# Optimization experiments

Hardware: AMD Instinct MI355X
Metric: run time of the kernel (lower is better)

Reference implementation:

```python
import jax, jax.numpy as jnp
import numpy as np

B, N, D, FF, L = 32, 1000, 128, 512, 6
EPS = 1e-5  # InstanceNorm1d default eps


def _inorm(x, g, b):
    # InstanceNorm1d on [B, d, N] == normalize over sequence dim N per channel (biased var)
    m = jnp.mean(x, axis=1, keepdims=True)
    v = jnp.var(x, axis=1, keepdims=True)
    return (x - m) / jnp.sqrt(v + EPS) * g + b


def setup_inputs() -> dict:
    key = jax.random.key(0)
    ks = jax.random.split(key, 10)
    s = 0.05
    data = jax.random.normal(ks[0], (B, N, 2), dtype=jnp.float32)
    # negative pairwise distances (module calls it negative_dist)
    dist = -jax.random.uniform(ks[1], (B, N, N), dtype=jnp.float32)
    log_scale = jnp.ones((1,), dtype=jnp.float32)
    We = jax.random.normal(ks[2], (D, 2), dtype=jnp.float32) * s
    be = jnp.zeros((D,), dtype=jnp.float32)
    Wq = jax.random.normal(ks[3], (L, D, D), dtype=jnp.float32) * s
    Wk = jax.random.normal(ks[4], (L, D, D), dtype=jnp.float32) * s
    Wv = jax.random.normal(ks[5], (L, D, D), dtype=jnp.float32) * s
    g1 = jnp.ones((L, D), dtype=jnp.float32)
    b1 = jnp.zeros((L, D), dtype=jnp.float32)
    W1 = jax.random.normal(ks[6], (L, FF, D), dtype=jnp.float32) * s
    bw1 = jnp.zeros((L, FF), dtype=jnp.float32)
    W2 = jax.random.normal(ks[7], (L, D, FF), dtype=jnp.float32) * s
    bw2 = jnp.zeros((L, D), dtype=jnp.float32)
    g2 = jnp.ones((L, D), dtype=jnp.float32)
    b2 = jnp.zeros((L, D), dtype=jnp.float32)
    alpha = jnp.ones((L,), dtype=jnp.float32)  # AFT_dist_alpha per layer
    return dict(data=data, dist=dist, log_scale=log_scale, We=We, be=be,
                Wq=Wq, Wk=Wk, Wv=Wv, g1=g1, b1=b1, W1=W1, bw1=bw1,
                W2=W2, bw2=bw2, g2=g2, b2=b2, alpha=alpha)


def reference(data, dist, log_scale, We, be, Wq, Wk, Wv, g1, b1, W1, bw1, W2, bw2, g2, b2, alpha):
    x = data @ We.T + be  # [B,N,D]
    for i in range(L):
        q = x @ Wq[i].T
        k = x @ Wk[i].T
        v = x @ Wv[i].T
        A = jnp.exp(log_scale[0] * alpha[i] * dist)  # [B,N,N]
        ek = jnp.exp(k)
        bias = jnp.einsum('bnm,bmd->bnd', A, ek * v)
        denom = jnp.einsum('bnm,bmd->bnd', A, ek)
        out = jax.nn.sigmoid(q) * (bias / denom)
        x1 = _inorm(x + out, g1[i], b1[i])
        h = jax.nn.relu(x1 @ W1[i].T + bw1[i]) @ W2[i].T + bw2[i]
        x = _inorm(x1 + h, g2[i], b2[i])
    return x
```

## Files before the change

### kernel.cpp

```cpp
#include <hip/hip_runtime.h>
#include <hip/hip_bf16.h>

typedef __attribute__((ext_vector_type(4))) float f32x4;
typedef __attribute__((ext_vector_type(8))) short bf16x8;
typedef __attribute__((ext_vector_type(4))) short s16x4;

#define LCOUNT 6

static __device__ __forceinline__ unsigned short f2b(float f){
  __hip_bfloat16 h = __float2bfloat16(f);
  return __builtin_bit_cast(unsigned short, h);
}
static __device__ __forceinline__ float b2f(unsigned short u){
  unsigned int x = ((unsigned int)u) << 16;
  return __builtin_bit_cast(float, x);
}
static __device__ __forceinline__ void gl16(const void* g, void* l){
  __builtin_amdgcn_global_load_lds(
      (const __attribute__((address_space(1))) void*)g,
      (__attribute__((address_space(3))) void*)l, 16, 0, 0);
}
static __device__ __forceinline__ f32x4 mfma16(bf16x8 a, bf16x8 b, f32x4 c){
  return __builtin_amdgcn_mfma_f32_16x16x32_bf16(a, b, c, 0, 0, 0);
}

__global__ void k_cvt5(const float* __restrict__ Wq, const float* __restrict__ Wk,
                       const float* __restrict__ Wv, const float* __restrict__ W1,
                       const float* __restrict__ W2,
                       unsigned short* __restrict__ wqb, unsigned short* __restrict__ wkb,
                       unsigned short* __restrict__ wvb, unsigned short* __restrict__ w1b,
                       unsigned short* __restrict__ w2b){
  int i = blockIdx.x*256 + threadIdx.x;
  if (i < 98304) wqb[i] = f2b(Wq[i]);
  else if (i < 196608) wkb[i-98304] = f2b(Wk[i-98304]);
  else if (i < 294912) wvb[i-196608] = f2b(Wv[i-196608]);
  else if (i < 688128) w1b[i-294912] = f2b(W1[i-294912]);
  else w2b[i-688128] = f2b(W2[i-688128]);
}

__global__ void k_cvtdist(const float* __restrict__ dist, unsigned short* __restrict__ db){
  int t = blockIdx.x*256 + threadIdx.x;
  int row = t >> 7, ch = t & 127;
  bf16x8 w;
  if (ch >= 125){
#pragma unroll
    for (int e=0;e<8;e++) w[e] = 0;
  } else {
    const float* p = dist + (size_t)row*1000 + ch*8;
    f32x4 a = *(const f32x4*)p;
    f32x4 b = *(const f32x4*)(p + 4);
#pragma unroll
    for (int e=0;e<4;e++){ w[e] = (short)f2b(a[e]); w[4+e] = (short)f2b(b[e]); }
  }
  *(bf16x8*)&db[(size_t)row*1024 + ch*8] = w;
}

__global__ void k_embed(const float* __restrict__ data, const float* __restrict__ We,
                        const float* __restrict__ be, float* __restrict__ x,
                        unsigned short* __restrict__ xb){
  int idx = blockIdx.x*256 + threadIdx.x;
  int d = idx & 127, bn = idx >> 7;
  float v = data[bn*2]*We[d*2] + data[bn*2+1]*We[d*2+1] + be[d];
  x[idx] = v; xb[idx] = f2b(v);
}

__global__ __launch_bounds__(256) void k_napply(
  const float* __restrict__ src, const float* __restrict__ part, int cnt,
  const float* __restrict__ g, const float* __restrict__ beta,
  float* __restrict__ dstf, unsigned short* __restrict__ dstb,
  float* __restrict__ dout)
{
  __shared__ float sna[128], snc[128];
  int blk = blockIdx.x, tid = threadIdx.x;
  int b = blk / 125;
  if (tid < 128){
    float s1 = 0.f, s2 = 0.f;
    for (int c = 0; c < cnt; ++c){
      size_t pi = (((size_t)b*cnt + c)*128 + tid)*2;
      s1 += part[pi]; s2 += part[pi+1];
    }
    float mean = s1 * 1e-3f;
    float var  = s2 * 1e-3f - mean*mean;
    float a = g[tid] * rsqrtf(var + 1e-5f);
    sna[tid] = a; snc[tid] = beta[tid] - mean*a;
  }
  __syncthreads();
  size_t base = (size_t)blk*1024 + tid*4;
  f32x4 v = *(const f32x4*)&src[base];
  int d0 = (tid*4) & 127;
  f32x4 o; s16x4 ob;
#pragma unroll
  for (int e=0;e<4;e++){
    o[e] = v[e]*sna[d0+e] + snc[d0+e];
    ob[e] = (short)f2b(o[e]);
  }
  *(f32x4*)&dstf[base] = o;
  *(s16x4*)&dstb[base] = ob;
  if (dout) *(f32x4*)&dout[base] = o;
}

__global__ __launch_bounds__(256) void k_qkv(
  const unsigned short* __restrict__ xb,
  const unsigned short* __restrict__ Wqb, const unsigned short* __restrict__ Wkb,
  const unsigned short* __restrict__ Wvb,
  unsigned short* __restrict__ sigq, unsigned short* __restrict__ Zc)
{
  __shared__ unsigned short LA[2][4][64][8];
  __shared__ unsigned short LB[2][4][256][8];
  int tid = threadIdx.x, wid = tid>>6, lane = tid&63;
  int l15 = lane&15, lg = lane>>4;
  int wm = wid>>1, wn = wid&1;
  int bt = blockIdx.x, b = bt>>4, t = bt&15;
  int kv = blockIdx.y;
  int lrow = t*64 + lane; if (lrow > 999) lrow = 999;
  size_t arow = (size_t)(b*1000 + lrow);

  f32x4 zf = {0.f,0.f,0.f,0.f};
  f32x4 acc[2][4], acc2[2][4];
#pragma unroll
  for (int i=0;i<2;i++)
#pragma unroll
    for (int j=0;j<4;j++){ acc[i][j] = zf; acc2[i][j] = zf; }

  auto stage = [&](int kk, int buf){
    int k0 = kk*32;
    gl16(xb + arow*128 + k0 + wid*8, &LA[buf][wid][0][0]);
    if (kv == 0){
#pragma unroll
      for (int t2=0;t2<2;++t2){
        int e = wid + t2*4, g2 = e>>1, nb = e&1;
        gl16(Wqb + (size_t)(nb*64+lane)*128 + k0 + g2*8, &LB[buf][g2][nb*64][0]);
      }
    } else {
#pragma unroll
      for (int t2=0;t2<4;++t2){
        int e = wid + t2*4, g2 = e&3, nb = e>>2;
        const unsigned short* src = (nb < 2)
          ? Wkb + (size_t)(nb*64+lane)*128 + k0 + g2*8
          : Wvb + (size_t)((nb-2)*64+lane)*128 + k0 + g2*8;
        gl16(src, &LB[buf][g2][nb*64][0]);
      }
    }
  };
  auto compute = [&](int buf){
    bf16x8 af[2];
#pragma unroll
    for (int i=0;i<2;i++) af[i] = *(const bf16x8*)&LA[buf][lg][wm*32 + i*16 + l15][0];
#pragma unroll
    for (int j=0;j<4;j++){
      bf16x8 bq = *(const bf16x8*)&LB[buf][lg][wn*64 + j*16 + l15][0];
#pragma unroll
      for (int i=0;i<2;i++) acc[i][j] = mfma16(af[i], bq, acc[i][j]);
      if (kv){
        bf16x8 bv = *(const bf16x8*)&LB[buf][lg][128 + wn*64 + j*16 + l15][0];
#pragma unroll
        for (int i=0;i<2;i++) acc2[i][j] = mfma16(af[i], bv, acc2[i][j]);
      }
    }
  };

  stage(0, 0);
  __syncthreads();
  for (int kk = 0; kk < 4; ++kk){
    int buf = kk & 1;
    if (kk < 3) stage(kk+1, buf^1);
    compute(buf);
    __syncthreads();
  }

#pragma unroll
  for (int i=0;i<2;i++){
    int m4 = t*64 + wm*32 + i*16 + lg*4;
    if (m4 >= 1000) continue;
#pragma unroll
    for (int j=0;j<4;j++){
      int col = wn*64 + j*16 + l15;
      if (kv == 0){
#pragma unroll
        for (int r=0;r<4;r++)
          sigq[(size_t)(b*1000 + m4 + r)*128 + col] = f2b(1.f/(1.f + __expf(-acc[i][j][r])));
      } else {
        s16x4 pv, pk;
#pragma unroll
        for (int r=0;r<4;r++){
          float ek = __expf(acc[i][j][r]);
          pk[r] = (short)f2b(ek);
          pv[r] = (short)f2b(ek * acc2[i][j][r]);
        }
        size_t base = ((size_t)(b*128 + (m4>>3))*256 + col)*8 + ((m4>>2)&1)*4;
        *(s16x4*)&Zc[base] = pv;
        *(s16x4*)&Zc[base + 1024] = pk;
      }
    }
  }
}

template<int USE16>
__global__ __launch_bounds__(256) void k_attn(
  const float* __restrict__ dist, const unsigned short* __restrict__ db16,
  const unsigned short* __restrict__ Zc, const unsigned short* __restrict__ sigq,
  float* __restrict__ x, float* __restrict__ partA,
  const float* __restrict__ log_scale, const float* __restrict__ alpha, int layer)
{
  union SM {
    struct { unsigned short A[2][4][64][8]; unsigned short B[2][4][256][8]; } st;
    float den[64][128];
  };
  __shared__ SM sm;
  int tid = threadIdx.x, wid = tid>>6, lane = tid&63;
  int l15 = lane&15, lg = lane>>4;
  int bb = blockIdx.y, t = blockIdx.x, n0 = t*64;
  float sc = log_scale[0]*alpha[layer];
  const unsigned short* Zb = Zc + ((size_t)bb << 18);
  int arow = tid>>2, ag = tid&3;
  int an = n0 + arow; if (an > 999) an = 999;
  const size_t drow = (size_t)(bb*1000 + an);

  f32x4 zf = {0.f,0.f,0.f,0.f};
  f32x4 acc[4][4];
#pragma unroll
  for (int i=0;i<4;i++)
#pragma unroll
    for (int j=0;j<4;j++) acc[i][j] = zf;

  auto issueB = [&](int kk, int buf){
#pragma unroll
    for (int t2=0;t2<4;++t2){
      int e = wid + t2*4, g2 = e&3, cb = e>>2;
      gl16(Zb + ((size_t)((kk*4 + g2)*256 + cb*64 + lane))*8, &sm.st.B[buf][g2][cb*64][0]);
    }
  };
  auto loadA = [&](int kk, float* v){
    int k0 = kk*32 + ag*8;
    if (USE16){
      bf16x8 r = *(const bf16x8*)(db16 + drow*1024 + k0);
#pragma unroll
      for (int e=0;e<8;e++) v[e] = b2f((unsigned short)r[e]);
    } else {
      const float* dp = dist + (size_t)drow*1000;
      if (k0 + 8 <= 1000){
        f32x4 a0 = *(const f32x4*)(dp + k0);
        f32x4 a1 = *(const f32x4*)(dp + k0 + 4);
#pragma unroll
        for (int e=0;e<4;e++){ v[e] = a0[e]; v[4+e] = a1[e]; }
      } else {
#pragma unroll
        for (int e=0;e<8;e++){
          int m = k0 + e; if (m > 999) m = 999;
          v[e] = dp[m];
        }
      }
    }
  };
  auto expwrite = [&](const float* v, int buf){
    bf16x8 w;
#pragma unroll
    for (int e=0;e<8;e++) w[e] = (short)f2b(__expf(sc*v[e]));
    *(bf16x8*)&sm.st.A[buf][ag][arow][0] = w;
  };
  auto compute = [&](int buf){
    bf16x8 af[4], bq[4];
#pragma unroll
    for (int i=0;i<4;i++) af[i] = *(const bf16x8*)&sm.st.A[buf][lg][i*16 + l15][0];
#pragma unroll
    for (int j=0;j<4;j++) bq[j] = *(const bf16x8*)&sm.st.B[buf][lg][wid*64 + j*16 + l15][0];
#pragma unroll
    for (int i=0;i<4;i++)
#pragma unroll
      for (int j=0;j<4;j++)
        acc[i][j] = mfma16(af[i], bq[j], acc[i][j]);
  };

  float av[8];
  issueB(0, 0);
  loadA(0, av);
  expwrite(av, 0);
  __syncthreads();
  for (int kk = 0; kk < 32; ++kk){
    int buf = kk & 1;
    float nv[8];
    if (kk < 31){ issueB(kk+1, buf^1); loadA(kk+1, nv); }
    compute(buf);
    if (kk < 31) expwrite(nv, buf^1);
    __syncthreads();
  }

  if (wid >= 2){
#pragma unroll
    for (int i=0;i<4;i++)
#pragma unroll
      for (int j=0;j<4;j++){
        int dcol = (wid-2)*64 + j*16 + l15;
#pragma unroll
        for (int r=0;r<4;r++)
          sm.den[i*16 + lg*4 + r][dcol] = acc[i][j][r];
      }
  }
  __syncthreads();
  if (wid < 2){
    float s1[4] = {0.f,0.f,0.f,0.f}, s2[4] = {0.f,0.f,0.f,0.f};
#pragma unroll
    for (int i=0;i<4;i++){
#pragma unroll
      for (int r=0;r<4;r++){
        int n = n0 + i*16 + lg*4 + r;
        if (n < 1000){
          size_t rowi = ((size_t)bb*1000 + n)*128;
#pragma unroll
          for (int j=0;j<4;j++){
            int d = wid*64 + j*16 + l15;
            float y = x[rowi + d] +
                      b2f(sigq[rowi + d]) * acc[i][j][r] / sm.den[i*16 + lg*4 + r][d];
            x[rowi + d] = y;
            s1[j] += y; s2[j] += y*y;
          }
        }
      }
    }
#pragma unroll
    for (int j=0;j<4;j++){
      s1[j] += __shfl_xor(s1[j], 16); s2[j] += __shfl_xor(s2[j], 16);
      s1[j] += __shfl_xor(s1[j], 32); s2[j] += __shfl_xor(s2[j], 32);
    }
    if (lg == 0){
#pragma unroll
      for (int j=0;j<4;j++){
        int d = wid*64 + j*16 + l15;
        size_t pi = (((size_t)bb*16 + t)*128 + d)*2;
        partA[pi] = s1[j]; partA[pi+1] = s2[j];
      }
    }
  }
}

__global__ __launch_bounds__(256) void k_ff1(
  const unsigned short* __restrict__ x1b, const unsigned short* __restrict__ W1b,
  const float* __restrict__ bw1, unsigned short* __restrict__ h1)
{
  __shared__ unsigned short LA[2][4][64][8];
  __shared__ unsigned short LB[2][4][128][8];
  int tid = threadIdx.x, wid = tid>>6, lane = tid&63;
  int l15 = lane&15, lg = lane>>4;
  int wm = wid>>1, wn = wid&1;
  int m0 = blockIdx.x*64, col0 = blockIdx.y*128;

  f32x4 zf = {0.f,0.f,0.f,0.f};
  f32x4 acc[2][4];
#pragma unroll
  for (int i=0;i<2;i++)
#pragma unroll
    for (int j=0;j<4;j++) acc[i][j] = zf;

  auto stage = [&](int kk, int buf){
    int k0 = kk*32;
    gl16(x1b + (size_t)(m0 + lane)*128 + k0 + wid*8, &LA[buf][wid][0][0]);
#pragma unroll
    for (int t2=0;t2<2;++t2){
      int e = wid + t2*4, g2 = e>>1, nb = e&1;
      gl16(W1b + (size_t)(col0 + nb*64 + lane)*128 + k0 + g2*8, &LB[buf][g2][nb*64][0]);
    }
  };
  auto compute = [&](int buf){
    bf16x8 af[2];
#pragma unroll
    for (int i=0;i<2;i++) af[i] = *(const bf16x8*)&LA[buf][lg][wm*32 + i*16 + l15][0];
#pragma unroll
    for (int j=0;j<4;j++){
      bf16x8 bq = *(const bf16x8*)&LB[buf][lg][wn*64 + j*16 + l15][0];
#pragma unroll
      for (int i=0;i<2;i++) acc[i][j] = mfma16(af[i], bq, acc[i][j]);
    }
  };

  stage(0, 0);
  __syncthreads();
  for (int kk = 0; kk < 4; ++kk){
    int buf = kk & 1;
    if (kk < 3) stage(kk+1, buf^1);
    compute(buf);
    __syncthreads();
  }

#pragma unroll
  for (int i=0;i<2;i++){
    int row0 = m0 + wm*32 + i*16 + lg*4;
#pragma unroll
    for (int j=0;j<4;j++){
      int col = col0 + wn*64 + j*16 + l15;
      float bz = bw1[col];
#pragma unroll
      for (int r=0;r<4;r++){
        float v = acc[i][j][r] + bz;
        h1[(size_t)(row0+r)*512 + col] = f2b(v > 0.f ? v : 0.f);
      }
    }
  }
}

__global__ __launch_bounds__(256) void k_ff2(
  const unsigned short* __restrict__ h1, const unsigned short* __restrict__ W2b,
  const float* __restrict__ bw2, const float* __restrict__ x1,
  float* __restrict__ x, float* __restrict__ partF)
{
  __shared__ unsigned short LA[2][4][64][8];
  __shared__ unsigned short LB[2][4][128][8];
  int tid = threadIdx.x, wid = tid>>6, lane = tid&63;
  int l15 = lane&15, lg = lane>>4;
  int wm = wid>>1, wn = wid&1;
  int bt = blockIdx.x, b = bt>>4, t = bt&15;
  int lrow = t*64 + lane; if (lrow > 999) lrow = 999;
  size_t arow = (size_t)(b*1000 + lrow);

  f32x4 zf = {0.f,0.f,0.f,0.f};
  f32x4 acc[2][4];
#pragma unroll
  for (int i=0;i<2;i++)
#pragma unroll
    for (int j=0;j<4;j++) acc[i][j] = zf;

  auto stage = [&](int kk, int buf){
    int k0 = kk*32;
    gl16(h1 + arow*512 + k0 + wid*8, &LA[buf][wid][0][0]);
#pragma unroll
    for (int t2=0;t2<2;++t2){
      int e = wid + t2*4, g2 = e>>1, nb = e&1;
      gl16(W2b + (size_t)(nb*64 + lane)*512 + k0 + g2*8, &LB[buf][g2][nb*64][0]);
    }
  };
  auto compute = [&](int buf){
    bf16x8 af[2];
#pragma unroll
    for (int i=0;i<2;i++) af[i] = *(const bf16x8*)&LA[buf][lg][wm*32 + i*16 + l15][0];
#pragma unroll
    for (int j=0;j<4;j++){
      bf16x8 bq = *(const bf16x8*)&LB[buf][lg][wn*64 + j*16 + l15][0];
#pragma unroll
      for (int i=0;i<2;i++) acc[i][j] = mfma16(af[i], bq, acc[i][j]);
    }
  };

  stage(0, 0);
  __syncthreads();
  for (int kk = 0; kk < 16; ++kk){
    int buf = kk & 1;
    if (kk < 15) stage(kk+1, buf^1);
    compute(buf);
    __syncthreads();
  }

  float s1[4] = {0.f,0.f,0.f,0.f}, s2[4] = {0.f,0.f,0.f,0.f};
#pragma unroll
  for (int i=0;i<2;i++){
    int m4 = t*64 + wm*32 + i*16 + lg*4;
    if (m4 >= 1000) continue;
#pragma unroll
    for (int j=0;j<4;j++){
      int col = wn*64 + j*16 + l15;
      float bz = bw2[col];
#pragma unroll
      for (int r=0;r<4;r++){
        size_t idx = (size_t)(b*1000 + m4 + r)*128 + col;
        float y = acc[i][j][r] + bz + x1[idx];
        x[idx] = y;
        s1[j] += y; s2[j] += y*y;
      }
    }
  }
#pragma unroll
  for (int j=0;j<4;j++){
    s1[j] += __shfl_xor(s1[j], 16); s2[j] += __shfl_xor(s2[j], 16);
    s1[j] += __shfl_xor(s1[j], 32); s2[j] += __shfl_xor(s2[j], 32);
  }
  if (lg == 0){
#pragma unroll
    for (int j=0;j<4;j++){
      int d = wn*64 + j*16 + l15;
      size_t pi = (((size_t)b*32 + t*2 + wm)*128 + d)*2;
      partF[pi] = s1[j]; partF[pi+1] = s2[j];
    }
  }
}

extern "C" void kernel_launch(void* const* d_in, const int* in_sizes, int n_in,
                              void* d_out, int out_size, void* d_ws, size_t ws_size,
                              hipStream_t stream) {
  const float* data = (const float*)d_in[0];
  const float* dist = (const float*)d_in[1];
  const float* log_scale = (const float*)d_in[2];
  const float* We = (const float*)d_in[3];
  const float* be = (const float*)d_in[4];
  const float* Wq = (const float*)d_in[5];
  const float* Wk = (const float*)d_in[6];
  const float* Wv = (const float*)d_in[7];
  const float* g1 = (const float*)d_in[8];
  const float* b1 = (const float*)d_in[9];
  const float* W1 = (const float*)d_in[10];
  const float* bw1 = (const float*)d_in[11];
  const float* W2 = (const float*)d_in[12];
  const float* bw2 = (const float*)d_in[13];
  const float* g2 = (const float*)d_in[14];
  const float* b2 = (const float*)d_in[15];
  const float* alpha = (const float*)d_in[16];
  float* dout = (float*)d_out;

  char* ws = (char*)d_ws;
  size_t off = 0;
  auto alloc = [&](size_t bytes) -> void* {
    void* p = ws + off; off += (bytes + 255) & ~(size_t)255; return p;
  };
  unsigned short* xb  = (unsigned short*)alloc(8192000);
  float* x            = (float*)alloc(16384000);
  unsigned short* sigq= (unsigned short*)alloc(8192000);
  unsigned short* Zc  = (unsigned short*)alloc(16777216);
  unsigned short* h1  = (unsigned short*)alloc(32768000);
  float* x1           = (float*)alloc(16384000);
  unsigned short* x1b = (unsigned short*)alloc(8192000);
  float* partA        = (float*)alloc(524288);
  float* partF        = (float*)alloc(1048576);
  unsigned short* wqb = (unsigned short*)alloc(196608);
  unsigned short* wkb = (unsigned short*)alloc(196608);
  unsigned short* wvb = (unsigned short*)alloc(196608);
  unsigned short* w1b = (unsigned short*)alloc(786432);
  unsigned short* w2b = (unsigned short*)alloc(786432);
  if (off > ws_size) return;
  unsigned short* db16p = nullptr;
  if (ws_size >= off + 131072256) db16p = (unsigned short*)alloc(131072000);

  hipMemsetAsync(Zc, 0, 16777216, stream);
  k_cvt5<<<4224, 256, 0, stream>>>(Wq, Wk, Wv, W1, W2, wqb, wkb, wvb, w1b, w2b);
  if (db16p) k_cvtdist<<<16000, 256, 0, stream>>>(dist, db16p);
  k_embed<<<16000, 256, 0, stream>>>(data, We, be, x, xb);

  for (int i = 0; i < LCOUNT; ++i){
    k_qkv<<<dim3(512,2), 256, 0, stream>>>(xb, wqb + i*16384, wkb + i*16384,
                                           wvb + i*16384, sigq, Zc);
    if (db16p)
      k_attn<1><<<dim3(16,32), 256, 0, stream>>>(dist, db16p, Zc, sigq, x, partA,
                                                 log_scale, alpha, i);
    else
      k_attn<0><<<dim3(16,32), 256, 0, stream>>>(dist, nullptr, Zc, sigq, x, partA,
                                                 log_scale, alpha, i);
    k_napply<<<4000, 256, 0, stream>>>(x, partA, 16, g1 + i*128, b1 + i*128,
                                       x1, x1b, nullptr);
    k_ff1<<<dim3(500,4), 256, 0, stream>>>(x1b, w1b + i*65536, bw1 + i*512, h1);
    k_ff2<<<512, 256, 0, stream>>>(h1, w2b + i*65536, bw2 + i*128, x1, x, partF);
    k_napply<<<4000, 256, 0, stream>>>(x, partF, 32, g2 + i*128, b2 + i*128,
                                       x, xb, (i == LCOUNT-1) ? dout : nullptr);
  }
}
```

Measured before the change: 964.6 us.

## Fuse first instance-norm into FF1 and halve attention row tile

After: 927.7 us. -3.8%, faster.

```diff
diff --git a/kernel.cpp b/kernel.cpp
--- a/kernel.cpp
+++ b/kernel.cpp
@@ -203,23 +203,23 @@
   const float* __restrict__ log_scale, const float* __restrict__ alpha, int layer)
 {
   union SM {
-    struct { unsigned short A[2][4][64][8]; unsigned short B[2][4][256][8]; } st;
-    float den[64][128];
+    struct { unsigned short A[2][4][32][8]; unsigned short B[2][4][256][8]; } st;
+    float den[32][128];
   };
   __shared__ SM sm;
   int tid = threadIdx.x, wid = tid>>6, lane = tid&63;
   int l15 = lane&15, lg = lane>>4;
-  int bb = blockIdx.y, t = blockIdx.x, n0 = t*64;
+  int bb = blockIdx.y, t = blockIdx.x, n0 = t*32;
   float sc = log_scale[0]*alpha[layer];
   const unsigned short* Zb = Zc + ((size_t)bb << 18);
-  int arow = tid>>2, ag = tid&3;
+  int arow = (tid>>2)&31, ag = tid&3;
   int an = n0 + arow; if (an > 999) an = 999;
   const size_t drow = (size_t)(bb*1000 + an);
 
   f32x4 zf = {0.f,0.f,0.f,0.f};
-  f32x4 acc[4][4];
-#pragma unroll
-  for (int i=0;i<4;i++)
+  f32x4 acc[2][4];
+#pragma unroll
+  for (int i=0;i<2;i++)
 #pragma unroll
     for (int j=0;j<4;j++) acc[i][j] = zf;
 
@@ -259,13 +259,13 @@
     *(bf16x8*)&sm.st.A[buf][ag][arow][0] = w;
   };
   auto compute = [&](int buf){
-    bf16x8 af[4], bq[4];
-#pragma unroll
-    for (int i=0;i<4;i++) af[i] = *(const bf16x8*)&sm.st.A[buf][lg][i*16 + l15][0];
+    bf16x8 af[2], bq[4];
+#pragma unroll
+    for (int i=0;i<2;i++) af[i] = *(const bf16x8*)&sm.st.A[buf][lg][i*16 + l15][0];
 #pragma unroll
     for (int j=0;j<4;j++) bq[j] = *(const bf16x8*)&sm.st.B[buf][lg][wid*64 + j*16 + l15][0];
 #pragma unroll
-    for (int i=0;i<4;i++)
+    for (int i=0;i<2;i++)
 #pragma unroll
       for (int j=0;j<4;j++)
         acc[i][j] = mfma16(af[i], bq[j], acc[i][j]);
@@ -273,21 +273,24 @@
 
   float av[8];
   issueB(0, 0);
-  loadA(0, av);
-  expwrite(av, 0);
+  if (tid < 128) loadA(0, av);
+  if (tid < 128) expwrite(av, 0);
   __syncthreads();
   for (int kk = 0; kk < 32; ++kk){
     int buf = kk & 1;
     float nv[8];
-    if (kk < 31){ issueB(kk+1, buf^1); loadA(kk+1, nv); }
+    if (kk < 31){
+      issueB(kk+1, buf^1);
+      if (tid < 128) loadA(kk+1, nv);
+    }
     compute(buf);
-    if (kk < 31) expwrite(nv, buf^1);
+    if (kk < 31 && tid < 128) expwrite(nv, buf^1);
     __syncthreads();
   }
 
   if (wid >= 2){
 #pragma unroll
-    for (int i=0;i<4;i++)
+    for (int i=0;i<2;i++)
 #pragma unroll
       for (int j=0;j<4;j++){
         int dcol = (wid-2)*64 + j*16 + l15;
@@ -300,7 +303,7 @@
   if (wid < 2){
     float s1[4] = {0.f,0.f,0.f,0.f}, s2[4] = {0.f,0.f,0.f,0.f};
 #pragma unroll
-    for (int i=0;i<4;i++){
+    for (int i=0;i<2;i++){
 #pragma unroll
       for (int r=0;r<4;r++){
         int n = n0 + i*16 + lg*4 + r;
@@ -326,38 +329,72 @@
 #pragma unroll
       for (int j=0;j<4;j++){
         int d = wid*64 + j*16 + l15;
-        size_t pi = (((size_t)bb*16 + t)*128 + d)*2;
+        size_t pi = (((size_t)bb*32 + t)*128 + d)*2;
         partA[pi] = s1[j]; partA[pi+1] = s2[j];
       }
     }
   }
 }
 
-__global__ __launch_bounds__(256) void k_ff1(
-  const unsigned short* __restrict__ x1b, const unsigned short* __restrict__ W1b,
-  const float* __restrict__ bw1, unsigned short* __restrict__ h1)
+__global__ __launch_bounds__(512) void k_ff1(
+  const float* __restrict__ x, const float* __restrict__ partA,
+  const float* __restrict__ g1, const float* __restrict__ b1,
+  const unsigned short* __restrict__ W1b, const float* __restrict__ bw1,
+  unsigned short* __restrict__ x1b, unsigned short* __restrict__ h1)
 {
   __shared__ unsigned short LA[2][4][64][8];
-  __shared__ unsigned short LB[2][4][128][8];
+  __shared__ unsigned short LB[2][4][512][8];
+  __shared__ float sna[128], snc[128];
   int tid = threadIdx.x, wid = tid>>6, lane = tid&63;
   int l15 = lane&15, lg = lane>>4;
-  int wm = wid>>1, wn = wid&1;
-  int m0 = blockIdx.x*64, col0 = blockIdx.y*128;
+  int wm = wid>>2, wn = wid&3;
+  int bt = blockIdx.x, b = bt>>4, t = bt&15;
+
+  if (tid < 128){
+    float s1 = 0.f, s2 = 0.f;
+    for (int c = 0; c < 32; ++c){
+      size_t pi = (((size_t)b*32 + c)*128 + tid)*2;
+      s1 += partA[pi]; s2 += partA[pi+1];
+    }
+    float mean = s1 * 1e-3f;
+    float var  = s2 * 1e-3f - mean*mean;
+    float a = g1[tid] * rsqrtf(var + 1e-5f);
+    sna[tid] = a; snc[tid] = b1[tid] - mean*a;
+  }
+  __syncthreads();
 
   f32x4 zf = {0.f,0.f,0.f,0.f};
-  f32x4 acc[2][4];
+  f32x4 acc[2][8];
 #pragma unroll
   for (int i=0;i<2;i++)
 #pragma unroll
-    for (int j=0;j<4;j++) acc[i][j] = zf;
+    for (int j=0;j<8;j++) acc[i][j] = zf;
 
   auto stage = [&](int kk, int buf){
     int k0 = kk*32;
-    gl16(x1b + (size_t)(m0 + lane)*128 + k0 + wid*8, &LA[buf][wid][0][0]);
-#pragma unroll
-    for (int t2=0;t2<2;++t2){
-      int e = wid + t2*4, g2 = e>>1, nb = e&1;
-      gl16(W1b + (size_t)(col0 + nb*64 + lane)*128 + k0 + g2*8, &LB[buf][g2][nb*64][0]);
+    if (tid < 256){
+      int row = tid>>2, g2 = tid&3;
+      int lr = t*64 + row;
+      int rr = lr > 999 ? 999 : lr;
+      const float* p = x + ((size_t)(b*1000 + rr))*128 + k0 + g2*8;
+      f32x4 v0 = *(const f32x4*)p;
+      f32x4 v1 = *(const f32x4*)(p + 4);
+      bf16x8 w;
+#pragma unroll
+      for (int e=0;e<4;e++){
+        int k = k0 + g2*8;
+        w[e]   = (short)f2b(v0[e]*sna[k+e]   + snc[k+e]);
+        w[4+e] = (short)f2b(v1[e]*sna[k+4+e] + snc[k+4+e]);
+      }
+      *(bf16x8*)&LA[buf][g2][row][0] = w;
+      if (lr < 1000)
+        *(bf16x8*)&x1b[((size_t)(b*1000 + lr))*128 + k0 + g2*8] = w;
+    }
+#pragma unroll
+    for (int t2=0;t2<4;++t2){
+      int e = wid*4 + t2;
+      int g2 = e & 3, nb = e >> 2;
+      gl16(W1b + (size_t)(nb*64 + lane)*128 + k0 + g2*8, &LB[buf][g2][nb*64][0]);
     }
   };
   auto compute = [&](int buf){
@@ -365,8 +402,8 @@
 #pragma unroll
     for (int i=0;i<2;i++) af[i] = *(const bf16x8*)&LA[buf][lg][wm*32 + i*16 + l15][0];
 #pragma unroll
-    for (int j=0;j<4;j++){
-      bf16x8 bq = *(const bf16x8*)&LB[buf][lg][wn*64 + j*16 + l15][0];
+    for (int j=0;j<8;j++){
+      bf16x8 bq = *(const bf16x8*)&LB[buf][lg][wn*128 + j*16 + l15][0];
 #pragma unroll
       for (int i=0;i<2;i++) acc[i][j] = mfma16(af[i], bq, acc[i][j]);
     }
@@ -383,15 +420,16 @@
 
 #pragma unroll
   for (int i=0;i<2;i++){
-    int row0 = m0 + wm*32 + i*16 + lg*4;
-#pragma unroll
-    for (int j=0;j<4;j++){
-      int col = col0 + wn*64 + j*16 + l15;
+    int m4 = t*64 + wm*32 + i*16 + lg*4;
+    if (m4 >= 1000) continue;
+#pragma unroll
+    for (int j=0;j<8;j++){
+      int col = wn*128 + j*16 + l15;
       float bz = bw1[col];
 #pragma unroll
       for (int r=0;r<4;r++){
         float v = acc[i][j][r] + bz;
-        h1[(size_t)(row0+r)*512 + col] = f2b(v > 0.f ? v : 0.f);
+        h1[(size_t)(b*1000 + m4 + r)*512 + col] = f2b(v > 0.f ? v : 0.f);
       }
     }
   }
@@ -399,7 +437,7 @@
 
 __global__ __launch_bounds__(256) void k_ff2(
   const unsigned short* __restrict__ h1, const unsigned short* __restrict__ W2b,
-  const float* __restrict__ bw2, const float* __restrict__ x1,
+  const float* __restrict__ bw2, const unsigned short* __restrict__ x1b,
   float* __restrict__ x, float* __restrict__ partF)
 {
   __shared__ unsigned short LA[2][4][64][8];
@@ -460,7 +498,7 @@
 #pragma unroll
       for (int r=0;r<4;r++){
         size_t idx = (size_t)(b*1000 + m4 + r)*128 + col;
-        float y = acc[i][j][r] + bz + x1[idx];
+        float y = acc[i][j][r] + bz + b2f(x1b[idx]);
         x[idx] = y;
         s1[j] += y; s2[j] += y*y;
       }
@@ -513,9 +551,8 @@
   unsigned short* sigq= (unsigned short*)alloc(8192000);
   unsigned short* Zc  = (unsigned short*)alloc(16777216);
   unsigned short* h1  = (unsigned short*)alloc(32768000);
-  float* x1           = (float*)alloc(16384000);
   unsigned short* x1b = (unsigned short*)alloc(8192000);
-  float* partA        = (float*)alloc(524288);
+  float* partA        = (float*)alloc(1048576);
   float* partF        = (float*)alloc(1048576);
   unsigned short* wqb = (unsigned short*)alloc(196608);
   unsigned short* wkb = (unsigned short*)alloc(196608);
@@ -535,15 +572,14 @@
     k_qkv<<<dim3(512,2), 256, 0, stream>>>(xb, wqb + i*16384, wkb + i*16384,
                                            wvb + i*16384, sigq, Zc);
     if (db16p)
-      k_attn<1><<<dim3(16,32), 256, 0, stream>>>(dist, db16p, Zc, sigq, x, partA,
+      k_attn<1><<<dim3(32,32), 256, 0, stream>>>(dist, db16p, Zc, sigq, x, partA,
                                                  log_scale, alpha, i);
     else
-      k_attn<0><<<dim3(16,32), 256, 0, stream>>>(dist, nullptr, Zc, sigq, x, partA,
+      k_attn<0><<<dim3(32,32), 256, 0, stream>>>(dist, nullptr, Zc, sigq, x, partA,
                                                  log_scale, alpha, i);
-    k_napply<<<4000, 256, 0, stream>>>(x, partA, 16, g1 + i*128, b1 + i*128,
-                                       x1, x1b, nullptr);
-    k_ff1<<<dim3(500,4), 256, 0, stream>>>(x1b, w1b + i*65536, bw1 + i*512, h1);
-    k_ff2<<<512, 256, 0, stream>>>(h1, w2b + i*65536, bw2 + i*128, x1, x, partF);
+    k_ff1<<<512, 512, 0, stream>>>(x, partA, g1 + i*128, b1 + i*128,
+                                   w1b + i*65536, bw1 + i*512, x1b, h1);
+    k_ff2<<<512, 256, 0, stream>>>(h1, w2b + i*65536, bw2 + i*128, x1b, x, partF);
     k_napply<<<4000, 256, 0, stream>>>(x, partF, 32, g2 + i*128, b2 + i*128,
                                        x, xb, (i == LCOUNT-1) ? dout : nullptr);
   }
```
